# Kernel tuning notes

Measured on AMD Instinct MI355X. Metric: run time of the kernel, lower is better.

The kernel has to match this reference:

```python
import jax, jax.numpy as jnp
import numpy as np

B, S, H, NH, HD = 1, 2048, 768, 12, 64   # batch, seq, hidden, heads, head_dim
W = 256                                   # one-sided window (attention_window=512)
NC = S // W                               # query chunks of width W
L, FF, V, G = 12, 3072, 50265, 1          # layers, ffn, vocab, num global tokens (CLS)
HID, EMB = 768, 256                       # head dense size, output embedding size
SCALE = 1.0 / np.sqrt(HD).astype(np.float32)
EPS = 1e-5

def _ln(x, s, b):
    mu = x.mean(-1, keepdims=True)
    xm = x - mu
    v = (xm * xm).mean(-1, keepdims=True)
    return xm * jax.lax.rsqrt(v + EPS) * s + b

def _forward(input_ids, attention_mask, global_attention_mask,
             word_emb, pos_emb, emb_ln_s, emb_ln_b,
             Wq, bq, Wk, bk, Wv, bv, Wqg, bqg, Wkg, bkg, Wvg, bvg, Wo, bo,
             ln1_s, ln1_b, Wf1, bf1, Wf2, bf2, ln2_s, ln2_b,
             dense_w, dense_b, out_w, out_b):
    h = word_emb[input_ids] + pos_emb[None]            # [B,S,H]
    h = _ln(h, emb_ln_s, emb_ln_b)

    key_ok = attention_mask.astype(bool)               # [B,S]
    is_glb = global_attention_mask.astype(bool)        # [B,S]

    # chunked sliding-window machinery: queries in NC chunks of W, each sees 3W keys
    j = jnp.arange(3 * W); qi = jnp.arange(W); c = jnp.arange(NC)
    rel = j[None, :] - qi[:, None]
    band_ok = (rel >= 0) & (rel <= 2 * W)              # |key-query| <= W  -> [W,3W]
    kpos = c[:, None, None] * W + j[None, None, :] - W # abs key position [NC,1,3W]
    in_range = (kpos >= 0) & (kpos < S)
    kposc = jnp.clip(kpos, 0, S - 1)
    # HF removes global tokens from the windowed band (they get dedicated columns)
    kmask = key_ok[:, kposc] & ~is_glb[:, kposc]       # [B,NC,1,3W]
    band_mask = band_ok[None, None] & in_range[None] & kmask          # [B,NC,W,3W]
    gcol_mask = jnp.broadcast_to(key_ok[:, None, None, :G], (B, NC, W, G))
    full_mask = jnp.concatenate([gcol_mask, band_mask], -1)[:, None]  # [B,1,NC,W,G+3W]
    kidx = c[:, None] * W + j[None, :]                 # gather into padded keys [NC,3W]

    def step(h, p):
        q = ((h @ p['Wq'] + p['bq']).reshape(B, NC, W, NH, HD)) * SCALE
        k = (h @ p['Wk'] + p['bk']).reshape(B, S, NH, HD)
        v = (h @ p['Wv'] + p['bv']).reshape(B, S, NH, HD)
        k_ch = jnp.pad(k, ((0, 0), (W, W), (0, 0), (0, 0)))[:, kidx]  # [B,NC,3W,NH,HD]
        v_ch = jnp.pad(v, ((0, 0), (W, W), (0, 0), (0, 0)))[:, kidx]
        s_band = jnp.einsum('bcqnd,bcknd->bncqk', q, k_ch)            # [B,NH,NC,W,3W]
        s_glob = jnp.einsum('bcqnd,bgnd->bncqg', q, k[:, :G])         # [B,NH,NC,W,G]
        scores = jnp.concatenate([s_glob, s_band], -1)
        probs = jax.nn.softmax(jnp.where(full_mask, scores, -1e9), -1)
        pg, pb = probs[..., :G], probs[..., G:]
        out = (jnp.einsum('bncqk,bcknd->bcqnd', pb, v_ch)
               + jnp.einsum('bncqg,bgnd->bcqnd', pg, v[:, :G]))
        out = out.reshape(B, S, NH, HD)
        # global tokens: full attention with dedicated global projections (HF semantics)
        hg = h[:, :G]
        qg = ((hg @ p['Wqg'] + p['bqg']).reshape(B, G, NH, HD)) * SCALE
        kg = (h @ p['Wkg'] + p['bkg']).reshape(B, S, NH, HD)
        vg = (h @ p['Wvg'] + p['bvg']).reshape(B, S, NH, HD)
        sg = jnp.einsum('bgnd,bsnd->bngs', qg, kg)
        ag = jax.nn.softmax(jnp.where(key_ok[:, None, None, :], sg, -1e9), -1)
        og = jnp.einsum('bngs,bsnd->bgnd', ag, vg)
        out = out.at[:, :G].set(og)
        attn = out.reshape(B, S, H) @ p['Wo'] + p['bo']
        h2 = _ln(h + attn, p['ln1_s'], p['ln1_b'])
        ff = jax.nn.gelu(h2 @ p['Wf1'] + p['bf1'], approximate=False) @ p['Wf2'] + p['bf2']
        return _ln(h2 + ff, p['ln2_s'], p['ln2_b']), None

    params = dict(Wq=Wq, bq=bq, Wk=Wk, bk=bk, Wv=Wv, bv=bv, Wqg=Wqg, bqg=bqg,
                  Wkg=Wkg, bkg=bkg, Wvg=Wvg, bvg=bvg, Wo=Wo, bo=bo,
                  ln1_s=ln1_s, ln1_b=ln1_b, Wf1=Wf1, bf1=bf1, Wf2=Wf2, bf2=bf2,
                  ln2_s=ln2_s, ln2_b=ln2_b)
    h, _ = jax.lax.scan(step, h, params)
    pooled = h[:, 0]                                   # CLS token
    y = jnp.tanh(pooled @ dense_w + dense_b)           # dropout = identity (eval)
    return y @ out_w + out_b                           # [B,EMB]

def setup_inputs() -> dict:
    key = jax.random.key(0)
    it = iter(jax.random.split(key, 16))
    def nrm(shape, sd=0.02):
        return jax.random.normal(next(it), shape, jnp.float32) * sd
    return dict(
        input_ids=jax.random.randint(next(it), (B, S), 0, V),
        attention_mask=jnp.ones((B, S), jnp.int32),
        global_attention_mask=jnp.zeros((B, S), jnp.int32).at[:, 0].set(1),
        word_emb=nrm((V, H)), pos_emb=nrm((S, H)),
        emb_ln_s=jnp.ones((H,)), emb_ln_b=jnp.zeros((H,)),
        Wq=nrm((L, H, H)), bq=jnp.zeros((L, H)),
        Wk=nrm((L, H, H)), bk=jnp.zeros((L, H)),
        Wv=nrm((L, H, H)), bv=jnp.zeros((L, H)),
        Wqg=nrm((L, H, H)), bqg=jnp.zeros((L, H)),
        Wkg=nrm((L, H, H)), bkg=jnp.zeros((L, H)),
        Wvg=nrm((L, H, H)), bvg=jnp.zeros((L, H)),
        Wo=nrm((L, H, H)), bo=jnp.zeros((L, H)),
        ln1_s=jnp.ones((L, H)), ln1_b=jnp.zeros((L, H)),
        Wf1=nrm((L, H, FF)), bf1=jnp.zeros((L, FF)),
        Wf2=nrm((L, FF, H)), bf2=jnp.zeros((L, H)),
        ln2_s=jnp.ones((L, H)), ln2_b=jnp.zeros((L, H)),
        dense_w=nrm((H, HID)), dense_b=jnp.zeros((HID,)),
        out_w=nrm((HID, EMB)), out_b=jnp.zeros((EMB,)),
    )

def reference(input_ids, attention_mask, global_attention_mask,
              word_emb, pos_emb, emb_ln_s, emb_ln_b,
              Wq, bq, Wk, bk, Wv, bv, Wqg, bqg, Wkg, bkg, Wvg, bvg, Wo, bo,
              ln1_s, ln1_b, Wf1, bf1, Wf2, bf2, ln2_s, ln2_b,
              dense_w, dense_b, out_w, out_b):
    return _forward(input_ids, attention_mask, global_attention_mask,
                    word_emb, pos_emb, emb_ln_s, emb_ln_b,
                    Wq, bq, Wk, bk, Wv, bv, Wqg, bqg, Wkg, bkg, Wvg, bvg, Wo, bo,
                    ln1_s, ln1_b, Wf1, bf1, Wf2, bf2, ln2_s, ln2_b,
                    dense_w, dense_b, out_w, out_b)
```

## Files before the change

### kernel.cpp

```cpp
#include <hip/hip_runtime.h>
#include <hip/hip_bf16.h>

typedef __hip_bfloat16 bf16;
using bf16x8 = __attribute__((ext_vector_type(8))) short;
using f32x4  = __attribute__((ext_vector_type(4))) float;

#define kNEG 1.0e9f

__device__ __forceinline__ float b2f(bf16 x){ return __bfloat162float(x); }
__device__ __forceinline__ bf16  f2b(float x){ return __float2bfloat16(x); }

#define GLDS16(gp, lp) __builtin_amdgcn_global_load_lds( \
    (const __attribute__((address_space(1))) void*)(gp), \
    (__attribute__((address_space(3))) void*)(lp), 16, 0, 0)

__device__ __forceinline__ void unpack8(uint4 u, float* f){
  f[0]=__uint_as_float(u.x<<16); f[1]=__uint_as_float(u.x&0xffff0000u);
  f[2]=__uint_as_float(u.y<<16); f[3]=__uint_as_float(u.y&0xffff0000u);
  f[4]=__uint_as_float(u.z<<16); f[5]=__uint_as_float(u.z&0xffff0000u);
  f[6]=__uint_as_float(u.w<<16); f[7]=__uint_as_float(u.w&0xffff0000u);
}

__global__ __launch_bounds__(256)
void embed_ln(const int* __restrict__ ids, const float* __restrict__ wemb,
              const float* __restrict__ pemb, const float* __restrict__ lns,
              const float* __restrict__ lnb, float* __restrict__ hout,
              bf16* __restrict__ hbout)
{
  const int row = blockIdx.x;
  const int tid = threadIdx.x;
  const int wave = tid >> 6, lane = tid & 63;
  const int id = ids[row];
  float x[3];
  #pragma unroll
  for (int p=0;p<3;p++){
    int i = tid + p*256;
    x[p] = wemb[(size_t)id*768 + i] + pemb[(size_t)row*768 + i];
  }
  float s1 = x[0]+x[1]+x[2];
  float s2 = x[0]*x[0]+x[1]*x[1]+x[2]*x[2];
  #pragma unroll
  for (int m=32;m>=1;m>>=1){ s1 += __shfl_xor(s1,m); s2 += __shfl_xor(s2,m); }
  __shared__ float red[8];
  if (lane==0){ red[wave]=s1; red[4+wave]=s2; }
  __syncthreads();
  s1 = red[0]+red[1]+red[2]+red[3];
  s2 = red[4]+red[5]+red[6]+red[7];
  float mu = s1*(1.0f/768.0f);
  float var = s2*(1.0f/768.0f) - mu*mu;
  float rs = rsqrtf(var + 1e-5f);
  #pragma unroll
  for (int p=0;p<3;p++){
    int i = tid + p*256;
    float y = (x[p]-mu)*rs*lns[i] + lnb[i];
    hout[(size_t)row*768+i] = y;
    hbout[(size_t)row*768+i] = f2b(y);
  }
}

__global__ __launch_bounds__(256)
void add_ln(const float* __restrict__ res, const bf16* __restrict__ pf,
            const float* __restrict__ lns, const float* __restrict__ lnb,
            float* __restrict__ hout, bf16* __restrict__ hbout)
{
  const size_t MN = (size_t)2048*768;
  const int row = blockIdx.x;
  const int tid = threadIdx.x;
  const int wave = tid >> 6, lane = tid & 63;
  float x[3];
  #pragma unroll
  for (int p=0;p<3;p++){
    int i = tid + p*256;
    size_t idx = (size_t)row*768+i;
    x[p] = res[idx] + ((b2f(pf[idx]) + b2f(pf[MN+idx]))
                     + (b2f(pf[2*MN+idx]) + b2f(pf[3*MN+idx])));
  }
  float s1 = x[0]+x[1]+x[2];
  float s2 = x[0]*x[0]+x[1]*x[1]+x[2]*x[2];
  #pragma unroll
  for (int m=32;m>=1;m>>=1){ s1 += __shfl_xor(s1,m); s2 += __shfl_xor(s2,m); }
  __shared__ float red[8];
  if (lane==0){ red[wave]=s1; red[4+wave]=s2; }
  __syncthreads();
  s1 = red[0]+red[1]+red[2]+red[3];
  s2 = red[4]+red[5]+red[6]+red[7];
  float mu = s1*(1.0f/768.0f);
  float var = s2*(1.0f/768.0f) - mu*mu;
  float rs = rsqrtf(var + 1e-5f);
  #pragma unroll
  for (int p=0;p<3;p++){
    int i = tid + p*256;
    float y = (x[p]-mu)*rs*lns[i] + lnb[i];
    hout[(size_t)row*768+i] = y;
    hbout[(size_t)row*768+i] = f2b(y);
  }
}

__global__ __launch_bounds__(256)
void prep_layer(const float* __restrict__ Wq, const float* __restrict__ Wk,
                const float* __restrict__ Wv, const float* __restrict__ Wkg,
                const float* __restrict__ Wvg, const float* __restrict__ Wo,
                const float* __restrict__ Wf1, const float* __restrict__ Wf2,
                const float* __restrict__ bq, const float* __restrict__ bk,
                const float* __restrict__ bv, const float* __restrict__ bkg,
                const float* __restrict__ bvg,
                bf16* __restrict__ WcatT, bf16* __restrict__ WoT,
                bf16* __restrict__ Wf1T, bf16* __restrict__ Wf2T,
                float* __restrict__ bcat, int l)
{
  const int b = blockIdx.x;
  const int tid = threadIdx.x;
  const size_t oHH = (size_t)l*768*768;
  const size_t oHF = (size_t)l*768*3072;
  const size_t oH  = (size_t)l*768;
  if (b >= 504) {
    int i = (b-504)*256 + tid;
    int which = i / 768, j = i - which*768;
    float v;
    if      (which==0) v = bq[oH+j] * 0.125f;
    else if (which==1) v = bk[oH+j];
    else if (which==2) v = bv[oH+j];
    else if (which==3) v = bkg[oH+j];
    else               v = bvg[oH+j];
    bcat[(size_t)l*3840 + i] = v;
    return;
  }
  const float* src; bf16* dst; int N, KT64, p0, tk, k0, n0; float scale = 1.0f;
  if (b < 180) {
    int wsel = b/36, tile = b - wsel*36;
    int tkk = tile/3, tn = tile - tkk*3;
    if      (wsel==0){ src=Wq+oHH;  scale=0.125f; }
    else if (wsel==1){ src=Wk+oHH; }
    else if (wsel==2){ src=Wv+oHH; }
    else if (wsel==3){ src=Wkg+oHH; }
    else             { src=Wvg+oHH; }
    dst = WcatT + (size_t)l*5*768*768;
    N=768; KT64=12; k0=tkk*64; n0=tn*256; p0 = wsel*6 + tn*2; tk = tkk;
  } else if (b < 216) {
    int tile = b-180, tkk = tile/3, tn = tile - tkk*3;
    src = Wo+oHH; dst = WoT + (size_t)l*768*768;
    N=768; KT64=12; k0=tkk*64; n0=tn*256; p0 = tn*2; tk = tkk;
  } else if (b < 360) {
    int tile = b-216, tkk = tile/12, tn = tile - tkk*12;
    src = Wf1+oHF; dst = Wf1T + (size_t)l*768*3072;
    N=3072; KT64=12; k0=tkk*64; n0=tn*256; p0 = tn*2; tk = tkk;
  } else {
    int tile = b-360, tkk = tile/3, tn = tile - tkk*3;
    src = Wf2+oHF; dst = Wf2T + (size_t)l*768*3072;
    N=768; KT64=48; k0=tkk*64; n0=tn*256; p0 = tn*2; tk = tkk;
  }

  __shared__ bf16 t[64][264];
  const int wave = tid>>6, lane = tid&63;
  float4 v[16];
  #pragma unroll
  for (int i=0;i<16;i++){
    int r = i*4 + wave;
    v[i] = *(const float4*)&src[(size_t)(k0+r)*N + n0 + lane*4];
  }
  #pragma unroll
  for (int i=0;i<16;i++){
    int r = i*4 + wave;
    union { ushort4 u; bf16 h[4]; } pk;
    pk.h[0]=f2b(v[i].x*scale); pk.h[1]=f2b(v[i].y*scale);
    pk.h[2]=f2b(v[i].z*scale); pk.h[3]=f2b(v[i].w*scale);
    *(ushort4*)&t[r][lane*4] = pk.u;
  }
  __syncthreads();
  const int rr = tid>>1, half = tid&1;
  const int r7 = rr & 7;
  #pragma unroll
  for (int c=0;c<4;c++){
    const int pp = c>>1, tt = c&1;
    union { uint4 u[2]; bf16 h[16]; } pk;
    #pragma unroll
    for (int j=0;j<16;j++)
      pk.h[j] = t[tt*32 + half*16 + j][pp*128 + rr];
    bf16* base = dst + ((size_t)(p0+pp)*KT64 + tk)*8192 + rr*64;
    const int g0 = tt*4 + half*2;
    *(uint4*)(base + (((g0  ) ^ r7)<<3)) = pk.u[0];
    *(uint4*)(base + (((g0+1) ^ r7)<<3)) = pk.u[1];
  }
}

template<int OUTF, int OUTB, int GELU, int KSPLIT, int VT>
__global__ __launch_bounds__(256)
void gemm_bt(const bf16* __restrict__ A, const bf16* __restrict__ Bt,
             const float* __restrict__ bias,
             bf16* __restrict__ pfb, bf16* __restrict__ outb,
             bf16* __restrict__ vt,
             int M, int N, int K)
{
  __shared__ bf16 As[2][128*64];
  __shared__ bf16 Bs[2][128*64];
  const int tid  = threadIdx.x;
  const int lane = tid & 63;
  const int wave = tid >> 6;
  const int wm = wave >> 1, wn = wave & 1;
  const int gx = gridDim.x, nwg = gx*gridDim.y;
  const int w  = blockIdx.y*gx + blockIdx.x;
  const int cpx = nwg >> 3;
  const int sw = (w & 7)*cpx + (w >> 3);
  const int bm = sw % gx, bn = sw / gx;
  const int bz = (KSPLIT>1) ? blockIdx.z : 0;
  const int fr = lane & 15;
  const int fk = lane >> 4;
  const int x7 = fr & 7;
  const int Ks = K / KSPLIT;
  const int nt = Ks >> 6;
  const int kbeg = bz * Ks;
  const int KT64 = K >> 6;

  const bf16* pa[4];
  int ldsA[4];
  #pragma unroll
  for (int i=0;i<4;i++){
    int s = i*256 + tid;
    int row = s >> 3, k8l = s & 7;
    pa[i] = A + (size_t)(bm*128 + row)*K + kbeg + ((k8l ^ (row&7))<<3);
    ldsA[i] = s*8;
  }
  const bf16* pB = Bt + ((size_t)bn*KT64 + (kbeg>>6))*8192;

  f32x4 acc[4][4];
  const f32x4 zero = {0.f,0.f,0.f,0.f};
  #pragma unroll
  for (int i=0;i<4;i++)
    #pragma unroll
    for (int j=0;j<4;j++) acc[i][j] = zero;

  #pragma unroll
  for (int i=0;i<4;i++) GLDS16(pa[i], &As[0][ldsA[i]]);
  #pragma unroll
  for (int i=0;i<4;i++){ int o=(i*256+tid)*8; GLDS16(pB+o, &Bs[0][o]); }
  if (nt > 1) {
    #pragma unroll
    for (int i=0;i<4;i++) GLDS16(pa[i]+64, &As[1][ldsA[i]]);
    #pragma unroll
    for (int i=0;i<4;i++){ int o=(i*256+tid)*8; GLDS16(pB+8192+o, &Bs[1][o]); }
  }

  for (int t = 0; t < nt; ++t) {
    const int cur = t & 1;
    if (t < nt-1) asm volatile("s_waitcnt vmcnt(8)" ::: "memory");
    else          asm volatile("s_waitcnt vmcnt(0)" ::: "memory");
    __builtin_amdgcn_s_barrier();
    __builtin_amdgcn_sched_barrier(0);

    bf16x8 af[2][4], bfr[2][4];
    #pragma unroll
    for (int kk=0;kk<2;kk++){
      #pragma unroll
      for (int m=0;m<4;m++)
        af[kk][m] = *reinterpret_cast<const bf16x8*>(
            &As[cur][(wm*64 + m*16 + fr)*64 + ((((kk<<2)+fk) ^ x7)<<3)]);
      #pragma unroll
      for (int n=0;n<4;n++)
        bfr[kk][n] = *reinterpret_cast<const bf16x8*>(
            &Bs[cur][(wn*64 + n*16 + fr)*64 + ((((kk<<2)+fk) ^ x7)<<3)]);
    }
    __builtin_amdgcn_s_setprio(1);
    #pragma unroll
    for (int kk=0;kk<2;kk++)
      #pragma unroll
      for (int m=0;m<4;m++)
        #pragma unroll
        for (int n=0;n<4;n++)
          acc[m][n] = __builtin_amdgcn_mfma_f32_16x16x32_bf16(af[kk][m], bfr[kk][n], acc[m][n], 0,0,0);
    __builtin_amdgcn_s_setprio(0);

    __builtin_amdgcn_s_barrier();
    __builtin_amdgcn_sched_barrier(0);
    if (t+2 < nt) {
      #pragma unroll
      for (int i=0;i<4;i++) GLDS16(pa[i] + (size_t)(t+2)*64, &As[cur][ldsA[i]]);
      #pragma unroll
      for (int i=0;i<4;i++){ int o=(i*256+tid)*8;
        GLDS16(pB + (size_t)(t+2)*8192 + o, &Bs[cur][o]); }
    }
  }

  const int row0 = bm*128 + wm*64 + (lane>>4)*4;
  const int col0 = bn*128 + wn*64 + fr;
  bf16* pfz = OUTF ? (pfb + (size_t)bz*M*N) : nullptr;
  #pragma unroll
  for (int n=0;n<4;n++){
    const int col = col0 + n*16;
    const float bv = (bz==0) ? bias[col] : 0.f;
    #pragma unroll
    for (int m=0;m<4;m++){
      const int r0 = row0 + m*16;
      union { ushort4 u; bf16 h[4]; } pk;
      #pragma unroll
      for (int r=0;r<4;r++){
        float x = acc[m][n][r] + bv;
        if (GELU) x = 0.5f*x*(1.0f + erff(x*0.70710678118f));
        size_t idx = (size_t)(r0+r)*N + col;
        pk.h[r] = f2b(x);
        if (OUTF) pfz[idx] = pk.h[r];
        if (OUTB) outb[idx] = pk.h[r];
      }
      if (VT) {
        if (col >= 1536 && col < 2304)
          *(ushort4*)&vt[(size_t)(col-1536)*2048 + r0] = pk.u;
      }
    }
  }
}

__global__ __launch_bounds__(256)
void band_attn(const bf16* __restrict__ qkv, const bf16* __restrict__ Vt,
               const float* __restrict__ h0, const float* __restrict__ Wqg,
               const float* __restrict__ bqg,
               const int* __restrict__ amask, const int* __restrict__ gmask,
               bf16* __restrict__ attn)
{
  const int c = blockIdx.x, n = blockIdx.y, rg = blockIdx.z;
  const int tid = threadIdx.x, wave = tid>>6, lane = tid&63;

  if (rg == 4) {
    if (c != 0) return;
    __shared__ float sg[2048];
    __shared__ float qh[64];
    __shared__ float redg[8];
    __shared__ float partg[4][64];
    {
      const int d = tid & 63;
      const int w = tid >> 6;
      const float* wp = Wqg + (size_t)(w*192)*768 + n*64 + d;
      float a = 0.f;
      #pragma unroll 8
      for (int k=0;k<192;k++) a += h0[w*192+k] * wp[(size_t)k*768];
      partg[w][d] = a;
    }
    __syncthreads();
    if (tid < 64)
      qh[tid] = (partg[0][tid]+partg[1][tid]+partg[2][tid]+partg[3][tid] + bqg[n*64+tid]) * 0.125f;
    __syncthreads();

    float smax = -3.0e38f;
    for (int p=0;p<8;p++){
      int s = p*256 + tid;
      const uint4* kr = (const uint4*)(qkv + (size_t)s*3840 + 2304 + n*64);
      float acc = 0.f;
      #pragma unroll
      for (int d8=0; d8<8; d8++){
        float f[8]; unpack8(kr[d8], f);
        #pragma unroll
        for (int e=0;e<8;e++) acc += f[e]*qh[d8*8+e];
      }
      if (amask[s] == 0) acc = -kNEG;
      sg[s] = acc;
      smax = fmaxf(smax, acc);
    }
    #pragma unroll
    for (int mk=32; mk>=1; mk>>=1) smax = fmaxf(smax, __shfl_xor(smax, mk));
    if (lane==0) redg[wave] = smax;
    __syncthreads();
    smax = fmaxf(fmaxf(redg[0],redg[1]),fmaxf(redg[2],redg[3]));
    float ssum = 0.f;
    for (int p=0;p<8;p++){
      int s = p*256 + tid;
      float e = __expf(sg[s]-smax);
      sg[s] = e;
      ssum += e;
    }
    #pragma unroll
    for (int mk=32; mk>=1; mk>>=1) ssum += __shfl_xor(ssum, mk);
    if (lane==0) redg[4+wave] = ssum;
    __syncthreads();
    float total = redg[4]+redg[5]+redg[6]+redg[7];
    __syncthreads();

    float o0=0.f,o1=0.f,o2=0.f,o3=0.f;
    const int base = wave*512;
    for (int s = base; s < base+512; s+=4){
      o0 += sg[s]   * b2f(qkv[(size_t)s*3840     + 3072 + n*64 + lane]);
      o1 += sg[s+1] * b2f(qkv[(size_t)(s+1)*3840 + 3072 + n*64 + lane]);
      o2 += sg[s+2] * b2f(qkv[(size_t)(s+2)*3840 + 3072 + n*64 + lane]);
      o3 += sg[s+3] * b2f(qkv[(size_t)(s+3)*3840 + 3072 + n*64 + lane]);
    }
    partg[wave][lane] = (o0+o1)+(o2+o3);
    __syncthreads();
    if (tid < 64) {
      float oo = (partg[0][tid]+partg[1][tid]+partg[2][tid]+partg[3][tid]) / total;
      attn[n*64+tid] = f2b(oo);
    }
    return;
  }

  const int fr = lane & 15, fk = lane >> 4;
  const int jj = tid >> 2, seg = tid & 3;

  __shared__ __attribute__((aligned(16))) bf16 q_s[64][72];
  __shared__ __attribute__((aligned(16))) bf16 k_s[2][64][72];
  __shared__ __attribute__((aligned(16))) bf16 vt_s[2][64][72];
  __shared__ __attribute__((aligned(16))) bf16 p_s[4][16][72];
  __shared__ int  okk_s[768];
  __shared__ float kv0[2][64];

  {
    const uint4* src = (const uint4*)(qkv + (size_t)(c*256 + rg*64 + jj)*3840 + n*64 + seg*16);
    *(uint4*)&q_s[jj][seg*16]   = src[0];
    *(uint4*)&q_s[jj][seg*16+8] = src[1];
  }
  #pragma unroll
  for (int p=0;p<3;p++){
    int j = tid + p*256;
    int kpos = c*256 + j - 256;
    int ok = 0;
    if (kpos >= 0 && kpos < 2048) ok = (amask[kpos] != 0) && (gmask[kpos] == 0);
    okk_s[j] = ok;
  }
  if (tid < 64)       kv0[0][tid]    = b2f(qkv[768  + n*64 + tid]);
  else if (tid < 128) kv0[1][tid-64] = b2f(qkv[1536 + n*64 + (tid-64)]);

  auto loadK = [&](int kt, uint4& a, uint4& b){
    int kpos = c*256 + kt*64 + jj - 256;
    int kq = kpos < 0 ? 0 : (kpos > 2047 ? 2047 : kpos);
    const uint4* ks = (const uint4*)(qkv + (size_t)kq*3840 + 768 + n*64 + seg*16);
    a = ks[0]; b = ks[1];
  };
  auto loadV = [&](int kt, uint4& a, uint4& b){
    int base = c*256 + kt*64 - 256;
    int sb = (base < 0 || base > 2048-64) ? 0 : base;
    const uint4* vs = (const uint4*)(Vt + (size_t)(n*64 + jj)*2048 + sb + seg*8);
    a = vs[0]; b = vs[4];
  };

  const int kt_lo = (c==0) ? ((rg > 4) ? rg : 4) : rg;
  int kt_hi = rg+8 < 11 ? rg+8 : 11;
  const int clip = (2303 - c*256) >> 6;
  if (kt_hi > clip) kt_hi = clip;

  uint4 ka,kb,va,vb;
  loadK(kt_lo,ka,kb); loadV(kt_lo,va,vb);
  *(uint4*)&k_s[0][jj][seg*16]    = ka;
  *(uint4*)&k_s[0][jj][seg*16+8]  = kb;
  *(uint4*)&vt_s[0][jj][seg*8]    = va;
  *(uint4*)&vt_s[0][jj][seg*8+32] = vb;

  float lsum[4];
  f32x4 out[4];
  const f32x4 zero = {0.f,0.f,0.f,0.f};
  #pragma unroll
  for (int r=0;r<4;r++) lsum[r] = 0.f;
  #pragma unroll
  for (int dt=0;dt<4;dt++) out[dt] = zero;

  int cur = 0;
  for (int kt = kt_lo; kt <= kt_hi; kt++) {
    const bool pf = (kt < kt_hi);
    if (pf){ loadK(kt+1,ka,kb); loadV(kt+1,va,vb); }
    __syncthreads();

    f32x4 s[4];
    #pragma unroll
    for (int ct=0;ct<4;ct++) s[ct] = zero;
    __builtin_amdgcn_s_setprio(1);
    #pragma unroll
    for (int ks=0;ks<2;ks++){
      bf16x8 aq = *reinterpret_cast<const bf16x8*>(&q_s[wave*16 + fr][ks*32 + fk*8]);
      #pragma unroll
      for (int ct=0;ct<4;ct++){
        bf16x8 bk = *reinterpret_cast<const bf16x8*>(&k_s[cur][ct*16 + fr][ks*32 + fk*8]);
        s[ct] = __builtin_amdgcn_mfma_f32_16x16x32_bf16(aq, bk, s[ct], 0,0,0);
      }
    }
    __builtin_amdgcn_s_setprio(0);
    const int qbase = rg*64 + wave*16 + fk*4;
    #pragma unroll
    for (int ct=0;ct<4;ct++){
      int j = kt*64 + ct*16 + fr;
      int okj = okk_s[j];
      #pragma unroll
      for (int r=0;r<4;r++){
        unsigned rel = (unsigned)(j - (qbase + r));
        float sv = (okj && rel <= 512u) ? s[ct][r] : -kNEG;
        float p = __expf(sv);
        lsum[r] += p;
        p_s[wave][fk*4 + r][ct*16 + fr] = f2b(p);
      }
    }
    __builtin_amdgcn_s_setprio(1);
    #pragma unroll
    for (int ks=0;ks<2;ks++){
      bf16x8 ap = *reinterpret_cast<const bf16x8*>(&p_s[wave][fr][ks*32 + fk*8]);
      #pragma unroll
      for (int dt=0;dt<4;dt++){
        bf16x8 bv = *reinterpret_cast<const bf16x8*>(&vt_s[cur][dt*16 + fr][ks*32 + fk*8]);
        out[dt] = __builtin_amdgcn_mfma_f32_16x16x32_bf16(ap, bv, out[dt], 0,0,0);
      }
    }
    __builtin_amdgcn_s_setprio(0);

    if (pf){
      *(uint4*)&k_s[cur^1][jj][seg*16]    = ka;
      *(uint4*)&k_s[cur^1][jj][seg*16+8]  = kb;
      *(uint4*)&vt_s[cur^1][jj][seg*8]    = va;
      *(uint4*)&vt_s[cur^1][jj][seg*8+32] = vb;
      cur ^= 1;
    }
  }

  const bool okg = (amask[0] != 0);
  #pragma unroll
  for (int r=0;r<4;r++){
    const int row16 = fk*4 + r;
    float ts = lsum[r];
    #pragma unroll
    for (int mk=8; mk>=1; mk>>=1) ts += __shfl_xor(ts, mk);
    float sp = 0.f;
    #pragma unroll
    for (int e=0;e<4;e++){
      int d = fr*4 + e;
      sp += b2f(q_s[wave*16 + row16][d]) * kv0[0][d];
    }
    #pragma unroll
    for (int mk=8; mk>=1; mk>>=1) sp += __shfl_xor(sp, mk);
    float pg = okg ? __expf(sp) : 0.f;
    float lf = ts + pg;
    const int srow = c*256 + rg*64 + wave*16 + row16;
    if (srow != 0) {
      #pragma unroll
      for (int dt=0;dt<4;dt++){
        int d = dt*16 + fr;
        float o = (out[dt][r] + pg*kv0[1][d]) / lf;
        attn[(size_t)srow*768 + n*64 + d] = f2b(o);
      }
    }
  }
}

__global__ __launch_bounds__(256)
void head_p1(const float* __restrict__ h0, const float* __restrict__ dw,
             float* __restrict__ pd)
{
  const int col = blockIdx.x*256 + threadIdx.x;
  const int z = blockIdx.y;
  const int k0 = z*96;
  float acc = 0.f;
  #pragma unroll 8
  for (int k=0;k<96;k++) acc += h0[k0+k]*dw[(size_t)(k0+k)*768 + col];
  pd[z*768 + col] = acc;
}

__global__ __launch_bounds__(256)
void head_y(const float* __restrict__ pd, const float* __restrict__ db,
            float* __restrict__ yv)
{
  const int col = blockIdx.x*256 + threadIdx.x;
  float a = 0.f;
  #pragma unroll
  for (int z=0;z<8;z++) a += pd[z*768 + col];
  yv[col] = tanhf(a + db[col]);
}

__global__ __launch_bounds__(256)
void head_p2(const float* __restrict__ yv, const float* __restrict__ ow,
             float* __restrict__ po)
{
  const int col = threadIdx.x;
  const int z = blockIdx.x;
  const int k0 = z*96;
  float acc = 0.f;
  #pragma unroll 8
  for (int k=0;k<96;k++) acc += yv[k0+k]*ow[(size_t)(k0+k)*256 + col];
  po[z*256 + col] = acc;
}

__global__ __launch_bounds__(256)
void head_fin(const float* __restrict__ po, const float* __restrict__ ob,
              float* __restrict__ out)
{
  const int col = threadIdx.x;
  float a = 0.f;
  #pragma unroll
  for (int z=0;z<8;z++) a += po[z*256 + col];
  out[col] = a + ob[col];
}

extern "C" void kernel_launch(void* const* d_in, const int* in_sizes, int n_in,
                              void* d_out, int out_size, void* d_ws, size_t ws_size,
                              hipStream_t stream)
{
  const int*   ids   = (const int*)d_in[0];
  const int*   amask = (const int*)d_in[1];
  const int*   gmask = (const int*)d_in[2];
  const float* wemb  = (const float*)d_in[3];
  const float* pemb  = (const float*)d_in[4];
  const float* elns  = (const float*)d_in[5];
  const float* elnb  = (const float*)d_in[6];
  const float* Wq    = (const float*)d_in[7];
  const float* bq    = (const float*)d_in[8];
  const float* Wk    = (const float*)d_in[9];
  const float* bk    = (const float*)d_in[10];
  const float* Wv    = (const float*)d_in[11];
  const float* bv    = (const float*)d_in[12];
  const float* Wqg   = (const float*)d_in[13];
  const float* bqg   = (const float*)d_in[14];
  const float* Wkg   = (const float*)d_in[15];
  const float* bkg   = (const float*)d_in[16];
  const float* Wvg   = (const float*)d_in[17];
  const float* bvg   = (const float*)d_in[18];
  const float* Wo    = (const float*)d_in[19];
  const float* bo    = (const float*)d_in[20];
  const float* ln1s  = (const float*)d_in[21];
  const float* ln1b  = (const float*)d_in[22];
  const float* Wf1   = (const float*)d_in[23];
  const float* bf1   = (const float*)d_in[24];
  const float* Wf2   = (const float*)d_in[25];
  const float* bf2   = (const float*)d_in[26];
  const float* ln2s  = (const float*)d_in[27];
  const float* ln2b  = (const float*)d_in[28];
  const float* dw    = (const float*)d_in[29];
  const float* db    = (const float*)d_in[30];
  const float* ow    = (const float*)d_in[31];
  const float* ob    = (const float*)d_in[32];

  char* ws = (char*)d_ws;
  size_t off = 0;
  auto alloc = [&](size_t bytes)->char*{
    char* p = ws + off; off += (bytes + 255) & ~(size_t)255; return p;
  };
  float* h     = (float*)alloc((size_t)2048*768*4);
  bf16*  hb    = (bf16*) alloc((size_t)2048*768*2);
  float* h2    = (float*)alloc((size_t)2048*768*4);
  bf16*  h2b   = (bf16*) alloc((size_t)2048*768*2);
  bf16*  qkv   = (bf16*) alloc((size_t)2048*3840*2);
  bf16*  att   = (bf16*) alloc((size_t)2048*768*2);
  bf16*  f1    = (bf16*) alloc((size_t)2048*3072*2);
  bf16*  Vtb   = (bf16*) alloc((size_t)768*2048*2);
  bf16*  pfb   = (bf16*) alloc((size_t)4*2048*768*2);
  bf16*  WcatT = (bf16*) alloc((size_t)12*5*768*768*2);
  bf16*  WoT   = (bf16*) alloc((size_t)12*768*768*2);
  bf16*  Wf1T  = (bf16*) alloc((size_t)12*768*3072*2);
  bf16*  Wf2T  = (bf16*) alloc((size_t)12*768*3072*2);
  float* bcat  = (float*)alloc((size_t)12*3840*4);
  float* pd    = (float*)alloc((size_t)8*768*4);
  float* yv    = (float*)alloc((size_t)768*4);
  float* po    = (float*)alloc((size_t)8*256*4);

  for (int l=0; l<12; l++)
    prep_layer<<<519,256,0,stream>>>(Wq, Wk, Wv, Wkg, Wvg, Wo, Wf1, Wf2,
                                     bq, bk, bv, bkg, bvg,
                                     WcatT, WoT, Wf1T, Wf2T, bcat, l);
  embed_ln<<<2048,256,0,stream>>>(ids, wemb, pemb, elns, elnb, h, hb);

  for (int l=0; l<12; l++) {
    const size_t oHH = (size_t)l*768*768;
    const size_t oH  = (size_t)l*768;
    const size_t oF  = (size_t)l*3072;
    const bf16* WcatT_l = WcatT + (size_t)l*5*768*768;
    const bf16* WoT_l   = WoT   + (size_t)l*768*768;
    const bf16* Wf1T_l  = Wf1T  + (size_t)l*768*3072;
    const bf16* Wf2T_l  = Wf2T  + (size_t)l*768*3072;
    const float* bcat_l = bcat  + (size_t)l*3840;

    gemm_bt<0,1,0,1,1><<<dim3(16,30),256,0,stream>>>(hb, WcatT_l, bcat_l, nullptr, qkv,
                                                     Vtb, 2048, 3840, 768);
    band_attn<<<dim3(8,12,5),256,0,stream>>>(qkv, Vtb, h, Wqg+oHH, bqg+oH,
                                             amask, gmask, att);
    gemm_bt<1,0,0,4,0><<<dim3(16,6,4),256,0,stream>>>(att, WoT_l, bo+oH, pfb, nullptr,
                                                      nullptr, 2048, 768, 768);
    add_ln<<<2048,256,0,stream>>>(h, pfb, ln1s+oH, ln1b+oH, h2, h2b);
    gemm_bt<0,1,1,1,0><<<dim3(16,24),256,0,stream>>>(h2b, Wf1T_l, bf1+oF, nullptr, f1,
                                                     nullptr, 2048, 3072, 768);
    gemm_bt<1,0,0,4,0><<<dim3(16,6,4),256,0,stream>>>(f1, Wf2T_l, bf2+oH, pfb, nullptr,
                                                      nullptr, 2048, 768, 3072);
    add_ln<<<2048,256,0,stream>>>(h2, pfb, ln2s+oH, ln2b+oH, h, hb);
  }

  head_p1<<<dim3(3,8),256,0,stream>>>(h, dw, pd);
  head_y<<<3,256,0,stream>>>(pd, db, yv);
  head_p2<<<8,256,0,stream>>>(yv, ow, po);
  head_fin<<<1,256,0,stream>>>(po, ob, (float*)d_out);
}
```

Before: 2.145 ms.

## Vectorize layernorm kernels, cut split-K to three, batch weight prep launch

The embedding and add+layernorm kernels now use 192 threads that each handle four contiguous elements with float4/ushort4 loads and stores, replacing scalar strided access. The Wo and Wf2 projections use three split-K partitions instead of four, so fewer partial buffers are written and later summed in add_ln. The twelve per-layer weight-prep launches become one 2D-grid launch. Fewer split-K partitions mean fewer blocks per GEMM, which may lower occupancy on those GEMMs.

```diff
diff --git a/kernel.cpp b/kernel.cpp
--- a/kernel.cpp
+++ b/kernel.cpp
@@ -9,6 +9,7 @@
 
 __device__ __forceinline__ float b2f(bf16 x){ return __bfloat162float(x); }
 __device__ __forceinline__ bf16  f2b(float x){ return __float2bfloat16(x); }
+__device__ __forceinline__ float us2f(unsigned short u){ return __uint_as_float(((unsigned)u)<<16); }
 
 #define GLDS16(gp, lp) __builtin_amdgcn_global_load_lds( \
     (const __attribute__((address_space(1))) void*)(gp), \
@@ -21,7 +22,7 @@
   f[6]=__uint_as_float(u.w<<16); f[7]=__uint_as_float(u.w&0xffff0000u);
 }
 
-__global__ __launch_bounds__(256)
+__global__ __launch_bounds__(192)
 void embed_ln(const int* __restrict__ ids, const float* __restrict__ wemb,
               const float* __restrict__ pemb, const float* __restrict__ lns,
               const float* __restrict__ lnb, float* __restrict__ hout,
@@ -31,34 +32,34 @@
   const int tid = threadIdx.x;
   const int wave = tid >> 6, lane = tid & 63;
   const int id = ids[row];
-  float x[3];
-  #pragma unroll
-  for (int p=0;p<3;p++){
-    int i = tid + p*256;
-    x[p] = wemb[(size_t)id*768 + i] + pemb[(size_t)row*768 + i];
-  }
-  float s1 = x[0]+x[1]+x[2];
-  float s2 = x[0]*x[0]+x[1]*x[1]+x[2]*x[2];
+  const int i0 = tid*4;
+  float4 a = *(const float4*)&wemb[(size_t)id*768 + i0];
+  float4 b = *(const float4*)&pemb[(size_t)row*768 + i0];
+  float4 x = make_float4(a.x+b.x, a.y+b.y, a.z+b.z, a.w+b.w);
+  float s1 = x.x+x.y+x.z+x.w;
+  float s2 = x.x*x.x+x.y*x.y+x.z*x.z+x.w*x.w;
   #pragma unroll
   for (int m=32;m>=1;m>>=1){ s1 += __shfl_xor(s1,m); s2 += __shfl_xor(s2,m); }
-  __shared__ float red[8];
-  if (lane==0){ red[wave]=s1; red[4+wave]=s2; }
+  __shared__ float red[6];
+  if (lane==0){ red[wave]=s1; red[3+wave]=s2; }
   __syncthreads();
-  s1 = red[0]+red[1]+red[2]+red[3];
-  s2 = red[4]+red[5]+red[6]+red[7];
+  s1 = red[0]+red[1]+red[2];
+  s2 = red[3]+red[4]+red[5];
   float mu = s1*(1.0f/768.0f);
   float var = s2*(1.0f/768.0f) - mu*mu;
   float rs = rsqrtf(var + 1e-5f);
-  #pragma unroll
-  for (int p=0;p<3;p++){
-    int i = tid + p*256;
-    float y = (x[p]-mu)*rs*lns[i] + lnb[i];
-    hout[(size_t)row*768+i] = y;
-    hbout[(size_t)row*768+i] = f2b(y);
-  }
-}
-
-__global__ __launch_bounds__(256)
+  float4 sc = *(const float4*)&lns[i0];
+  float4 bi = *(const float4*)&lnb[i0];
+  float4 y = make_float4((x.x-mu)*rs*sc.x + bi.x, (x.y-mu)*rs*sc.y + bi.y,
+                         (x.z-mu)*rs*sc.z + bi.z, (x.w-mu)*rs*sc.w + bi.w);
+  *(float4*)&hout[(size_t)row*768 + i0] = y;
+  union { ushort4 u; bf16 h[4]; } pk;
+  pk.h[0]=f2b(y.x); pk.h[1]=f2b(y.y); pk.h[2]=f2b(y.z); pk.h[3]=f2b(y.w);
+  *(ushort4*)&hbout[(size_t)row*768 + i0] = pk.u;
+}
+
+template<int NP>
+__global__ __launch_bounds__(192)
 void add_ln(const float* __restrict__ res, const bf16* __restrict__ pf,
             const float* __restrict__ lns, const float* __restrict__ lnb,
             float* __restrict__ hout, bf16* __restrict__ hbout)
@@ -67,48 +68,50 @@
   const int row = blockIdx.x;
   const int tid = threadIdx.x;
   const int wave = tid >> 6, lane = tid & 63;
-  float x[3];
-  #pragma unroll
-  for (int p=0;p<3;p++){
-    int i = tid + p*256;
-    size_t idx = (size_t)row*768+i;
-    x[p] = res[idx] + ((b2f(pf[idx]) + b2f(pf[MN+idx]))
-                     + (b2f(pf[2*MN+idx]) + b2f(pf[3*MN+idx])));
-  }
-  float s1 = x[0]+x[1]+x[2];
-  float s2 = x[0]*x[0]+x[1]*x[1]+x[2]*x[2];
+  const int i0 = tid*4;
+  const size_t base = (size_t)row*768 + i0;
+  float4 x = *(const float4*)&res[base];
+  #pragma unroll
+  for (int p=0;p<NP;p++){
+    ushort4 u = *(const ushort4*)&pf[p*MN + base];
+    x.x += us2f(u.x); x.y += us2f(u.y); x.z += us2f(u.z); x.w += us2f(u.w);
+  }
+  float s1 = x.x+x.y+x.z+x.w;
+  float s2 = x.x*x.x+x.y*x.y+x.z*x.z+x.w*x.w;
   #pragma unroll
   for (int m=32;m>=1;m>>=1){ s1 += __shfl_xor(s1,m); s2 += __shfl_xor(s2,m); }
-  __shared__ float red[8];
-  if (lane==0){ red[wave]=s1; red[4+wave]=s2; }
+  __shared__ float red[6];
+  if (lane==0){ red[wave]=s1; red[3+wave]=s2; }
   __syncthreads();
-  s1 = red[0]+red[1]+red[2]+red[3];
-  s2 = red[4]+red[5]+red[6]+red[7];
+  s1 = red[0]+red[1]+red[2];
+  s2 = red[3]+red[4]+red[5];
   float mu = s1*(1.0f/768.0f);
   float var = s2*(1.0f/768.0f) - mu*mu;
   float rs = rsqrtf(var + 1e-5f);
-  #pragma unroll
-  for (int p=0;p<3;p++){
-    int i = tid + p*256;
-    float y = (x[p]-mu)*rs*lns[i] + lnb[i];
-    hout[(size_t)row*768+i] = y;
-    hbout[(size_t)row*768+i] = f2b(y);
-  }
+  float4 sc = *(const float4*)&lns[i0];
+  float4 bi = *(const float4*)&lnb[i0];
+  float4 y = make_float4((x.x-mu)*rs*sc.x + bi.x, (x.y-mu)*rs*sc.y + bi.y,
+                         (x.z-mu)*rs*sc.z + bi.z, (x.w-mu)*rs*sc.w + bi.w);
+  *(float4*)&hout[base] = y;
+  union { ushort4 u; bf16 h[4]; } pk;
+  pk.h[0]=f2b(y.x); pk.h[1]=f2b(y.y); pk.h[2]=f2b(y.z); pk.h[3]=f2b(y.w);
+  *(ushort4*)&hbout[base] = pk.u;
 }
 
 __global__ __launch_bounds__(256)
-void prep_layer(const float* __restrict__ Wq, const float* __restrict__ Wk,
-                const float* __restrict__ Wv, const float* __restrict__ Wkg,
-                const float* __restrict__ Wvg, const float* __restrict__ Wo,
-                const float* __restrict__ Wf1, const float* __restrict__ Wf2,
-                const float* __restrict__ bq, const float* __restrict__ bk,
-                const float* __restrict__ bv, const float* __restrict__ bkg,
-                const float* __restrict__ bvg,
-                bf16* __restrict__ WcatT, bf16* __restrict__ WoT,
-                bf16* __restrict__ Wf1T, bf16* __restrict__ Wf2T,
-                float* __restrict__ bcat, int l)
+void prep_all(const float* __restrict__ Wq, const float* __restrict__ Wk,
+              const float* __restrict__ Wv, const float* __restrict__ Wkg,
+              const float* __restrict__ Wvg, const float* __restrict__ Wo,
+              const float* __restrict__ Wf1, const float* __restrict__ Wf2,
+              const float* __restrict__ bq, const float* __restrict__ bk,
+              const float* __restrict__ bv, const float* __restrict__ bkg,
+              const float* __restrict__ bvg,
+              bf16* __restrict__ WcatT, bf16* __restrict__ WoT,
+              bf16* __restrict__ Wf1T, bf16* __restrict__ Wf2T,
+              float* __restrict__ bcat)
 {
   const int b = blockIdx.x;
+  const int l = blockIdx.y;
   const int tid = threadIdx.x;
   const size_t oHH = (size_t)l*768*768;
   const size_t oHF = (size_t)l*768*3072;
@@ -641,11 +644,10 @@
   float* yv    = (float*)alloc((size_t)768*4);
   float* po    = (float*)alloc((size_t)8*256*4);
 
-  for (int l=0; l<12; l++)
-    prep_layer<<<519,256,0,stream>>>(Wq, Wk, Wv, Wkg, Wvg, Wo, Wf1, Wf2,
-                                     bq, bk, bv, bkg, bvg,
-                                     WcatT, WoT, Wf1T, Wf2T, bcat, l);
-  embed_ln<<<2048,256,0,stream>>>(ids, wemb, pemb, elns, elnb, h, hb);
+  prep_all<<<dim3(519,12),256,0,stream>>>(Wq, Wk, Wv, Wkg, Wvg, Wo, Wf1, Wf2,
+                                          bq, bk, bv, bkg, bvg,
+                                          WcatT, WoT, Wf1T, Wf2T, bcat);
+  embed_ln<<<2048,192,0,stream>>>(ids, wemb, pemb, elns, elnb, h, hb);
 
   for (int l=0; l<12; l++) {
     const size_t oHH = (size_t)l*768*768;
@@ -661,14 +663,14 @@
                                                      Vtb, 2048, 3840, 768);
     band_attn<<<dim3(8,12,5),256,0,stream>>>(qkv, Vtb, h, Wqg+oHH, bqg+oH,
                                              amask, gmask, att);
-    gemm_bt<1,0,0,4,0><<<dim3(16,6,4),256,0,stream>>>(att, WoT_l, bo+oH, pfb, nullptr,
+    gemm_bt<1,0,0,3,0><<<dim3(16,6,3),256,0,stream>>>(att, WoT_l, bo+oH, pfb, nullptr,
                                                       nullptr, 2048, 768, 768);
-    add_ln<<<2048,256,0,stream>>>(h, pfb, ln1s+oH, ln1b+oH, h2, h2b);
+    add_ln<3><<<2048,192,0,stream>>>(h, pfb, ln1s+oH, ln1b+oH, h2, h2b);
     gemm_bt<0,1,1,1,0><<<dim3(16,24),256,0,stream>>>(h2b, Wf1T_l, bf1+oF, nullptr, f1,
                                                      nullptr, 2048, 3072, 768);
-    gemm_bt<1,0,0,4,0><<<dim3(16,6,4),256,0,stream>>>(f1, Wf2T_l, bf2+oH, pfb, nullptr,
+    gemm_bt<1,0,0,3,0><<<dim3(16,6,3),256,0,stream>>>(f1, Wf2T_l, bf2+oH, pfb, nullptr,
                                                       nullptr, 2048, 768, 3072);
-    add_ln<<<2048,256,0,stream>>>(h2, pfb, ln2s+oH, ln2b+oH, h, hb);
+    add_ln<3><<<2048,192,0,stream>>>(h2, pfb, ln2s+oH, ln2b+oH, h, hb);
   }
 
   head_p1<<<dim3(3,8),256,0,stream>>>(h, dw, pd);
```

Measured after the change: 2.137 ms. No clear change (-0.4%).
